# Performance work log

Hardware: AMD Instinct MI355X
Metric: run time of the kernel (lower is better)

Reference implementation:

```python
import jax, jax.numpy as jnp
import numpy as np

RENORM_PERIOD = 256
MAX_NORM = 100.0


def setup_inputs() -> dict:
    key = jax.random.key(0)
    ks = jax.random.split(key, 9)
    B, S, G, D, N = 4, 2048, 8, 128, 64
    return {
        "x_r": jax.random.normal(ks[0], (B, S, G, D), jnp.float32),
        "x_i": jax.random.normal(ks[1], (B, S, G, D), jnp.float32),
        "log_A_mag": jax.random.uniform(ks[2], (G, N), jnp.float32) * 0.5 + 0.5,
        "A_phase": jax.random.normal(ks[3], (G, N), jnp.float32) * 0.1,
        "Bw_r": jax.random.normal(ks[4], (N, D), jnp.float32) / np.sqrt(D),
        "Bw_i": jax.random.normal(ks[5], (N, D), jnp.float32) / np.sqrt(D),
        "Cw_r": jax.random.normal(ks[6], (D, N), jnp.float32) / np.sqrt(N),
        "Cw_i": jax.random.normal(ks[7], (D, N), jnp.float32) / np.sqrt(N),
        "dt_w": jax.random.normal(ks[8], (2, 2 * D), jnp.float32) * 0.02,
        "dt_b": jnp.zeros((2,), jnp.float32),
    }


def reference(x_r, x_i, log_A_mag, A_phase, Bw_r, Bw_i, Cw_r, Cw_i, dt_w, dt_b):
    B, S, G, D = x_r.shape
    N = Bw_r.shape[0]
    # dt: input-dependent step magnitude / phase scale, clamped
    x_cat = jnp.concatenate([x_r, x_i], axis=-1)            # [B,S,G,2D]
    dt = jnp.clip(jnp.exp(jnp.einsum('bsgd,od->bsgo', x_cat, dt_w) + dt_b), 1e-4, 2.0)
    dt_mag = dt[..., 0:1]                                    # [B,S,G,1]
    dt_phase = dt[..., 1:2]
    # A_bar in polar form, |A| = exp(-softplus(log_A_mag)*dt_mag) < 1
    neg_log_A = -jax.nn.softplus(log_A_mag)[None, None]      # [1,1,G,N]
    A_mag = jnp.exp(dt_mag * neg_log_A)                      # [B,S,G,N]
    A_ang = dt_phase * A_phase[None, None]
    A_r = A_mag * jnp.cos(A_ang)
    A_i = A_mag * jnp.sin(A_ang)
    # Bx = (B_proj @ x) * dt_mag, complex linear
    Bx_r = (jnp.einsum('bsgd,nd->bsgn', x_r, Bw_r) - jnp.einsum('bsgd,nd->bsgn', x_i, Bw_i)) * dt_mag
    Bx_i = (jnp.einsum('bsgd,nd->bsgn', x_r, Bw_i) + jnp.einsum('bsgd,nd->bsgn', x_i, Bw_r)) * dt_mag

    def step(carry, inp):
        h_r, h_i = carry
        ar, ai, br, bi, t = inp
        nh_r = ar * h_r - ai * h_i + br
        nh_i = ar * h_i + ai * h_r + bi
        renorm = ((t + 1) % RENORM_PERIOD) == 0
        norm = jnp.sqrt(nh_r * nh_r + nh_i * nh_i + 1e-8)
        scale = jnp.minimum(norm, MAX_NORM) / norm
        nh_r = jnp.where(renorm, nh_r * scale, nh_r)
        nh_i = jnp.where(renorm, nh_i * scale, nh_i)
        return (nh_r, nh_i), (nh_r, nh_i)

    h0 = (jnp.zeros((B, G, N), jnp.float32), jnp.zeros((B, G, N), jnp.float32))
    xs = (jnp.moveaxis(A_r, 1, 0), jnp.moveaxis(A_i, 1, 0),
          jnp.moveaxis(Bx_r, 1, 0), jnp.moveaxis(Bx_i, 1, 0),
          jnp.arange(S))
    _, (all_h_r, all_h_i) = jax.lax.scan(step, h0, xs)       # [S,B,G,N]
    all_h_r = jnp.moveaxis(all_h_r, 0, 1)                    # [B,S,G,N]
    all_h_i = jnp.moveaxis(all_h_i, 0, 1)
    # y = C_proj(h), complex linear N -> D
    y_r = jnp.einsum('bsgn,dn->bsgd', all_h_r, Cw_r) - jnp.einsum('bsgn,dn->bsgd', all_h_i, Cw_i)
    y_i = jnp.einsum('bsgn,dn->bsgd', all_h_r, Cw_i) + jnp.einsum('bsgn,dn->bsgd', all_h_i, Cw_r)
    return jnp.stack([y_r, y_i], axis=0)                     # [2,B,S,G,D]
```

## Files before the change

### kernel.cpp

```cpp
#include <hip/hip_runtime.h>
#include <math.h>

#define B_ 4
#define S_ 2048
#define G_ 8
#define D_ 128
#define N_ 64
#define ROWS (B_*S_*G_)
#define CH 64
#define CLEN 32
#define YOFF (ROWS*D_)

typedef short bf16x8 __attribute__((ext_vector_type(8)));
typedef float f32x4  __attribute__((ext_vector_type(4)));
#define MFMA16(a,b,c) __builtin_amdgcn_mfma_f32_16x16x32_bf16(a,b,c,0,0,0)

__device__ __forceinline__ unsigned short bf16_rtne(float f) {
    unsigned u = __float_as_uint(f);
    unsigned r = (u + 0x7FFFu + ((u >> 16) & 1u)) >> 16;
    return (unsigned short)r;
}
__device__ __forceinline__ void split_bf16(float f, unsigned short &hi, unsigned short &lo) {
    hi = bf16_rtne(f);
    float hif = __uint_as_float(((unsigned)hi) << 16);
    lo = bf16_rtne(f - hif);
}
__device__ __forceinline__ unsigned pk_bf16(float a, float b) {
    unsigned r;
    asm("v_cvt_pk_bf16_f32 %0, %1, %2" : "=v"(r) : "v"(a), "v"(b));
    return r;
}
__device__ __forceinline__ float dot4(float4 a, float4 b) {
    return fmaf(a.x,b.x, fmaf(a.y,b.y, fmaf(a.z,b.z, a.w*b.w)));
}

__global__ __launch_bounds__(256) void k_prep(
    const float* __restrict__ bwr, const float* __restrict__ bwi,
    const float* __restrict__ cwr, const float* __restrict__ cwi,
    unsigned short* __restrict__ wbhi, unsigned short* __restrict__ wblo,
    unsigned short* __restrict__ wchi)
{
    int tid = blockIdx.x * 256 + threadIdx.x;
    if (tid < 4096) {
        int f = tid;
        int lane = f & 63, ks = (f >> 6) & 7, nt = (f >> 9) & 1, w = f >> 10;
        int l15 = lane & 15, quad = lane >> 4;
        int n = w * 32 + nt * 16 + l15;
        int k0 = ks * 32 + quad * 8;
        const float* src; float sgn = 1.f;
        if (n < 64) {
            if (k0 < 128) src = bwr + n * 128 + k0;
            else        { src = bwi + n * 128 + (k0 - 128); sgn = -1.f; }
        } else {
            if (k0 < 128) src = bwi + (n - 64) * 128 + k0;
            else          src = bwr + (n - 64) * 128 + (k0 - 128);
        }
        float4 v0 = *(const float4*)src;
        float4 v1 = *(const float4*)(src + 4);
        float vv[8] = {v0.x,v0.y,v0.z,v0.w,v1.x,v1.y,v1.z,v1.w};
        unsigned short h[8], l[8];
        #pragma unroll
        for (int j = 0; j < 8; j++) split_bf16(vv[j] * sgn, h[j], l[j]);
        #pragma unroll
        for (int j = 0; j < 8; j++) { wbhi[f*8+j] = h[j]; wblo[f*8+j] = l[j]; }
    } else {
        int f = tid - 4096;
        int lane = f & 63, ks = (f >> 6) & 3, nt = (f >> 8) & 3, w = f >> 10;
        int l15 = lane & 15, quad = lane >> 4;
        int n = w * 64 + nt * 16 + l15;
        int d = (n < 128) ? n : (n - 128);
        int k0 = ks * 32 + quad * 8;
        unsigned short h[8];
        #pragma unroll
        for (int j = 0; j < 8; j++) {
            int k = k0 + j, col = k >> 1;
            float val;
            if (n < 128) val = (k & 1) ? -cwi[d * 64 + col] : cwr[d * 64 + col];
            else         val = (k & 1) ?  cwr[d * 64 + col] : cwi[d * 64 + col];
            unsigned short hh, hl; split_bf16(val, hh, hl);
            h[j] = hh;
        }
        #pragma unroll
        for (int j = 0; j < 8; j++) wchi[f*8+j] = h[j];
    }
}

#define LDK1 264
__global__ __launch_bounds__(256, 8) void k_g1(
    const float* __restrict__ xr, const float* __restrict__ xi,
    const float* __restrict__ dtw, const float* __restrict__ dtb,
    const float* __restrict__ logAm, const float* __restrict__ Aph,
    const unsigned short* __restrict__ wbhi,
    float* __restrict__ bxr, float* __restrict__ bxi,
    float* __restrict__ dt_mag, float* __restrict__ dt_ph,
    float4* __restrict__ trans)
{
    __shared__ __align__(16) unsigned short Ahi[32 * LDK1];
    __shared__ float4 comb[192];
    __shared__ float dms[32], dps[32];
    float* bxs = (float*)Ahi;
    const int t = threadIdx.x;
    const int lane = t & 63, w = t >> 6;
    const int l15 = lane & 15, quad = lane >> 4;
    const int bg = blockIdx.x >> 6, c = blockIdx.x & 63;
    const int g = bg & 7, b = bg >> 3;
    const int crow = (bg * CH + c) * CLEN;

    const int kq = t & 31, k4 = kq * 4;
    float4 w0r = *(const float4*)(dtw + k4);
    float4 w0i = *(const float4*)(dtw + 128 + k4);
    float4 w1r = *(const float4*)(dtw + 256 + k4);
    float4 w1i = *(const float4*)(dtw + 384 + k4);
    float b0 = dtb[0], b1 = dtb[1];
    float nla = -logf(1.0f + __expf(logAm[g * N_ + lane]));
    float aph = Aph[g * N_ + lane];

    const bf16x8* WHp = (const bf16x8*)wbhi + (w * 2) * 512 + lane;
    bf16x8 wh0 = WHp[0];
    bf16x8 wh1 = WHp[512];

    const int s0 = c * CLEN;
    const float* xrb = xr + ((size_t)(b * S_ + s0) * G_ + g) * 128;
    const float* xib = xi + ((size_t)(b * S_ + s0) * G_ + g) * 128;

    float pm[4], pp[4];
    #pragma unroll
    for (int i = 0; i < 4; i++) {
        int f = t + 256 * i;
        int m = f >> 5, kk = f & 31;
        float4 a  = ((const float4*)(xrb + m * 1024))[kk];
        float4 bb = ((const float4*)(xib + m * 1024))[kk];
        uint2 h2;
        h2 = make_uint2(pk_bf16(a.x, a.y), pk_bf16(a.z, a.w));
        *(uint2*)&Ahi[m * LDK1 + kk * 4] = h2;
        h2 = make_uint2(pk_bf16(bb.x, bb.y), pk_bf16(bb.z, bb.w));
        *(uint2*)&Ahi[m * LDK1 + 128 + kk * 4] = h2;
        pm[i] = dot4(a, w0r) + dot4(bb, w0i);
        pp[i] = dot4(a, w1r) + dot4(bb, w1i);
    }
    #pragma unroll
    for (int i = 0; i < 4; i++) {
        float vm = pm[i], vp = pp[i];
        #pragma unroll
        for (int msk = 16; msk >= 1; msk >>= 1) {
            vm += __shfl_xor(vm, msk);
            vp += __shfl_xor(vp, msk);
        }
        if ((t & 31) == 0) {
            int m = (t >> 5) + 8 * i;
            float dm = fminf(fmaxf(__expf(vm + b0), 1e-4f), 2.0f);
            float dp = fminf(fmaxf(__expf(vp + b1), 1e-4f), 2.0f);
            dms[m] = dm; dps[m] = dp;
            dt_mag[crow + m] = dm; dt_ph[crow + m] = dp;
        }
    }
    __syncthreads();

    f32x4 acc[2][2];
    #pragma unroll
    for (int a = 0; a < 2; a++)
        #pragma unroll
        for (int bq = 0; bq < 2; bq++)
            acc[a][bq] = (f32x4){0.f, 0.f, 0.f, 0.f};
    #pragma unroll
    for (int ks = 0; ks < 8; ks++) {
        bf16x8 nh0, nh1;
        if (ks < 7) {
            nh0 = WHp[(ks + 1) * 64];
            nh1 = WHp[512 + (ks + 1) * 64];
        }
        #pragma unroll
        for (int ms = 0; ms < 2; ms++) {
            int arow = (ms * 16 + l15) * LDK1 + quad * 8;
            bf16x8 ah = *(const bf16x8*)&Ahi[arow + ks * 32];
            acc[ms][0] = MFMA16(ah, wh0, acc[ms][0]);
            acc[ms][1] = MFMA16(ah, wh1, acc[ms][1]);
        }
        if (ks < 7) { wh0 = nh0; wh1 = nh1; }
    }
    __syncthreads();

    #pragma unroll
    for (int ms = 0; ms < 2; ms++)
        #pragma unroll
        for (int nt = 0; nt < 2; nt++) {
            int n = w * 32 + nt * 16 + l15;
            float* dstg = (n < 64) ? bxr : bxi;
            int nn = n & 63;
            #pragma unroll
            for (int r = 0; r < 4; r++) {
                int m = ms * 16 + quad * 4 + r;
                float v = acc[ms][nt][r] * dms[m];
                dstg[(crow + m) * 64 + nn] = v;
                bxs[m * 132 + n] = v;
            }
        }
    __syncthreads();

    {
        float Ar = 1.f, Ai = 0.f, Br = 0.f, Bi = 0.f;
        const int base = w * 8;
        #pragma unroll
        for (int tt = 0; tt < 8; tt++) {
            const int m = base + tt;
            float dm = dms[m], dp = dps[m];
            float am  = __expf(dm * nla);
            float ang = dp * aph;
            float cr = am * __cosf(ang), ci = am * __sinf(ang);
            float vr = bxs[m * 132 + lane], vi = bxs[m * 132 + 64 + lane];
            float nAr = cr * Ar - ci * Ai;
            float nAi = cr * Ai + ci * Ar;
            float nBr = cr * Br - ci * Bi + vr;
            float nBi = cr * Bi + ci * Br + vi;
            Ar = nAr; Ai = nAi; Br = nBr; Bi = nBi;
        }
        if (w < 3) comb[w * 64 + lane] = make_float4(Ar, Ai, Br, Bi);
        __syncthreads();
        if (w == 3) {
            float4 c0 = comb[lane];
            float cAr = c0.x, cAi = c0.y, cBr = c0.z, cBi = c0.w;
            #pragma unroll
            for (int s = 1; s < 3; s++) {
                float4 ps = comb[s * 64 + lane];
                float nAr = ps.x * cAr - ps.y * cAi;
                float nAi = ps.x * cAi + ps.y * cAr;
                float nBr = ps.x * cBr - ps.y * cBi + ps.z;
                float nBi = ps.x * cBi + ps.y * cBr + ps.w;
                cAr = nAr; cAi = nAi; cBr = nBr; cBi = nBi;
            }
            float fAr = Ar * cAr - Ai * cAi;
            float fAi = Ar * cAi + Ai * cAr;
            float fBr = Ar * cBr - Ai * cBi + Br;
            float fBi = Ar * cBi + Ai * cBr + Bi;
            trans[(bg * CH + c) * 64 + lane] = make_float4(fAr, fAi, fBr, fBi);
        }
    }
}

__global__ __launch_bounds__(256) void k_scanB2(const float4* __restrict__ trans,
    float2* __restrict__ hstart)
{
    int w = threadIdx.x >> 6, lane = threadIdx.x & 63;
    int W = blockIdx.x * 4 + w;
    int bg = W >> 3;
    int n  = ((W & 7) << 3) + (lane & 7);
    int j  = lane >> 3;
    float pAr[8], pAi[8], pBr[8], pBi[8];
    float Ar = 1.f, Ai = 0.f, Br = 0.f, Bi = 0.f;
    const float4* tp = trans + (bg * CH + j * 8) * 64 + n;
    #pragma unroll
    for (int k = 0; k < 8; k++) {
        pAr[k] = Ar; pAi[k] = Ai; pBr[k] = Br; pBi[k] = Bi;
        float4 T = tp[k * 64];
        float nAr = T.x * Ar - T.y * Ai;
        float nAi = T.x * Ai + T.y * Ar;
        float nBr = T.x * Br - T.y * Bi + T.z;
        float nBi = T.x * Bi + T.y * Br + T.w;
        Ar = nAr; Ai = nAi; Br = nBr; Bi = nBi;
    }
    float hr = 0.f, hi = 0.f, mhr = 0.f, mhi = 0.f;
    #pragma unroll
    for (int j2 = 0; j2 < 8; j2++) {
        if (j2 == j) { mhr = hr; mhi = hi; }
        int src = j2 * 8 + (lane & 7);
        float sAr = __shfl(Ar, src), sAi = __shfl(Ai, src);
        float sBr = __shfl(Br, src), sBi = __shfl(Bi, src);
        float nr = sAr * hr - sAi * hi + sBr;
        float ni = sAr * hi + sAi * hr + sBi;
        float nrm = sqrtf(nr * nr + ni * ni + 1e-8f);
        float sc = fminf(nrm, 100.f) / nrm;
        hr = nr * sc; hi = ni * sc;
    }
    float2* hp = hstart + (bg * CH + j * 8) * 64 + n;
    #pragma unroll
    for (int k = 0; k < 8; k++) {
        float hsr = pAr[k] * mhr - pAi[k] * mhi + pBr[k];
        float hsi = pAr[k] * mhi + pAi[k] * mhr + pBi[k];
        hp[k * 64] = make_float2(hsr, hsi);
    }
}

#define LDK2 152
__global__ __launch_bounds__(256, 6) void k_sg2(
    const float* __restrict__ bxr, const float* __restrict__ bxi,
    const float* __restrict__ dt_mag, const float* __restrict__ dt_ph,
    const float* __restrict__ logAm, const float* __restrict__ Aph,
    const float2* __restrict__ hstart,
    const unsigned short* __restrict__ wchi,
    float* __restrict__ out)
{
    __shared__ __align__(16) unsigned short Ahi[32 * LDK2];
    __shared__ __align__(16) unsigned short Alo[32 * LDK2];
    const int t = threadIdx.x;
    const int lane = t & 63, w = t >> 6;
    const int l15 = lane & 15, quad = lane >> 4;
    const int bg = blockIdx.x >> 6, c = blockIdx.x & 63;
    const int g = bg & 7, b = bg >> 3;

    if (w == 0) {
        const int n = lane;
        float nla = -logf(1.0f + __expf(logAm[g * N_ + n]));
        float aph = Aph[g * N_ + n];
        float2 h0 = hstart[(bg * CH + c) * 64 + n];
        float hr = h0.x, hi = h0.y;
        const bool rn = ((c & 7) == 7);
        const int base = (bg * CH + c) * CLEN;
        #pragma unroll 8
        for (int tt = 0; tt < CLEN; tt++) {
            float dm = dt_mag[base + tt], dp = dt_ph[base + tt];
            float am  = __expf(dm * nla);
            float ang = dp * aph;
            float cr = am * __cosf(ang), ci = am * __sinf(ang);
            float vr = bxr[(base + tt) * 64 + n];
            float vi = bxi[(base + tt) * 64 + n];
            float nr = cr * hr - ci * hi + vr;
            float ni = cr * hi + ci * hr + vi;
            if (rn && tt == CLEN - 1) {
                float nrm = sqrtf(nr * nr + ni * ni + 1e-8f);
                float scale = fminf(nrm, 100.0f) / nrm;
                nr *= scale; ni *= scale;
            }
            hr = nr; hi = ni;
            unsigned hp = pk_bf16(hr, hi);
            float rr = hr - __uint_as_float(hp << 16);
            float ri = hi - __uint_as_float(hp & 0xFFFF0000u);
            unsigned lp = pk_bf16(rr, ri);
            *(unsigned*)&Ahi[tt * LDK2 + 2 * n] = hp;
            *(unsigned*)&Alo[tt * LDK2 + 2 * n] = lp;
        }
    }
    __syncthreads();

    f32x4 acc[2][4];
    #pragma unroll
    for (int a = 0; a < 2; a++)
        #pragma unroll
        for (int bq = 0; bq < 4; bq++)
            acc[a][bq] = (f32x4){0.f, 0.f, 0.f, 0.f};
    #pragma unroll
    for (int ks = 0; ks < 4; ks++) {
        bf16x8 wc0 = ((const bf16x8*)wchi)[((w * 4 + 0) * 4 + ks) * 64 + lane];
        bf16x8 wc1 = ((const bf16x8*)wchi)[((w * 4 + 1) * 4 + ks) * 64 + lane];
        bf16x8 wc2 = ((const bf16x8*)wchi)[((w * 4 + 2) * 4 + ks) * 64 + lane];
        bf16x8 wc3 = ((const bf16x8*)wchi)[((w * 4 + 3) * 4 + ks) * 64 + lane];
        #pragma unroll
        for (int ms = 0; ms < 2; ms++) {
            int arow = (ms * 16 + l15) * LDK2 + quad * 8;
            bf16x8 ah = *(const bf16x8*)&Ahi[arow + ks * 32];
            bf16x8 al = *(const bf16x8*)&Alo[arow + ks * 32];
            acc[ms][0] = MFMA16(al, wc0, acc[ms][0]);
            acc[ms][0] = MFMA16(ah, wc0, acc[ms][0]);
            acc[ms][1] = MFMA16(al, wc1, acc[ms][1]);
            acc[ms][1] = MFMA16(ah, wc1, acc[ms][1]);
            acc[ms][2] = MFMA16(al, wc2, acc[ms][2]);
            acc[ms][2] = MFMA16(ah, wc2, acc[ms][2]);
            acc[ms][3] = MFMA16(al, wc3, acc[ms][3]);
            acc[ms][3] = MFMA16(ah, wc3, acc[ms][3]);
        }
    }
    #pragma unroll
    for (int ms = 0; ms < 2; ms++)
        #pragma unroll
        for (int nt = 0; nt < 4; nt++) {
            int nn = w * 64 + nt * 16 + l15;
            float* dst = (nn < 128) ? (out + nn) : (out + YOFF + (nn - 128));
            #pragma unroll
            for (int r = 0; r < 4; r++) {
                int tt2 = ms * 16 + quad * 4 + r;
                int srow = (b * S_ + c * CLEN + tt2) * G_ + g;
                dst[srow * 128] = acc[ms][nt][r];
            }
        }
}

extern "C" void kernel_launch(void* const* d_in, const int* in_sizes, int n_in,
                              void* d_out, int out_size, void* d_ws, size_t ws_size,
                              hipStream_t stream) {
    (void)in_sizes; (void)n_in; (void)out_size; (void)ws_size;
    const float* xr    = (const float*)d_in[0];
    const float* xi    = (const float*)d_in[1];
    const float* logAm = (const float*)d_in[2];
    const float* Aph   = (const float*)d_in[3];
    const float* bwr   = (const float*)d_in[4];
    const float* bwi   = (const float*)d_in[5];
    const float* cwr   = (const float*)d_in[6];
    const float* cwi   = (const float*)d_in[7];
    const float* dtw   = (const float*)d_in[8];
    const float* dtb   = (const float*)d_in[9];
    float* out = (float*)d_out;
    float* ws  = (float*)d_ws;

    float*  dt_mag = ws;
    float*  dt_ph  = ws + 65536;
    float*  bxr    = ws + 131072;
    float*  bxi    = bxr + 4194304;
    float4* trans  = (float4*)(ws + 8519680);
    float2* hstart = (float2*)(ws + 9043968);
    unsigned short* wbhi = (unsigned short*)(ws + 9306112);
    unsigned short* wblo = wbhi + 32768;
    unsigned short* wchi = wblo + 32768;

    hipLaunchKernelGGL(k_prep,   dim3(32), dim3(256), 0, stream,
                       bwr, bwi, cwr, cwi, wbhi, wblo, wchi);
    hipLaunchKernelGGL(k_g1,     dim3((B_ * G_) * 64), dim3(256), 0, stream,
                       xr, xi, dtw, dtb, logAm, Aph, wbhi,
                       bxr, bxi, dt_mag, dt_ph, trans);
    hipLaunchKernelGGL(k_scanB2, dim3(64), dim3(256), 0, stream,
                       trans, hstart);
    hipLaunchKernelGGL(k_sg2,    dim3((B_ * G_) * 64), dim3(256), 0, stream,
                       bxr, bxi, dt_mag, dt_ph, logAm, Aph, hstart, wchi, out);
}
```

Before: 168.4 us.

## Pack Bx to bf16 pairs, two chunks per g1 block, 4-wave parallel chunk scan

Bx is now stored as packed bf16 real/imag pairs instead of two fp32 arrays, halving intermediate write and read traffic. k_g1 handles two consecutive chunks per block and prefetches both chunks' x data into registers up front, which raises per-thread register use and lowers the launch-bounds occupancy target. The final scan kernel splits each 32-step chunk across four waves using local prefix products plus a cross-wave combine, replacing the single-wave serial recurrence. Rounding Bx to bf16 lowers the precision of the scan inputs.

```diff
diff --git a/kernel.cpp b/kernel.cpp
--- a/kernel.cpp
+++ b/kernel.cpp
@@ -86,25 +86,25 @@
 }
 
 #define LDK1 264
-__global__ __launch_bounds__(256, 8) void k_g1(
+__global__ __launch_bounds__(256, 4) void k_g1(
     const float* __restrict__ xr, const float* __restrict__ xi,
     const float* __restrict__ dtw, const float* __restrict__ dtb,
     const float* __restrict__ logAm, const float* __restrict__ Aph,
     const unsigned short* __restrict__ wbhi,
-    float* __restrict__ bxr, float* __restrict__ bxi,
+    unsigned* __restrict__ bxp,
     float* __restrict__ dt_mag, float* __restrict__ dt_ph,
     float4* __restrict__ trans)
 {
     __shared__ __align__(16) unsigned short Ahi[32 * LDK1];
     __shared__ float4 comb[192];
-    __shared__ float dms[32], dps[32];
+    __shared__ float dms[64], dps[64];
     float* bxs = (float*)Ahi;
     const int t = threadIdx.x;
     const int lane = t & 63, w = t >> 6;
     const int l15 = lane & 15, quad = lane >> 4;
-    const int bg = blockIdx.x >> 6, c = blockIdx.x & 63;
+    const int bg = blockIdx.x >> 5, cp = blockIdx.x & 31;
     const int g = bg & 7, b = bg >> 3;
-    const int crow = (bg * CH + c) * CLEN;
+    const int c0 = cp * 2;
 
     const int kq = t & 31, k4 = kq * 4;
     float4 w0r = *(const float4*)(dtw + k4);
@@ -116,123 +116,142 @@
     float aph = Aph[g * N_ + lane];
 
     const bf16x8* WHp = (const bf16x8*)wbhi + (w * 2) * 512 + lane;
-    bf16x8 wh0 = WHp[0];
-    bf16x8 wh1 = WHp[512];
-
-    const int s0 = c * CLEN;
-    const float* xrb = xr + ((size_t)(b * S_ + s0) * G_ + g) * 128;
-    const float* xib = xi + ((size_t)(b * S_ + s0) * G_ + g) * 128;
-
-    float pm[4], pp[4];
-    #pragma unroll
-    for (int i = 0; i < 4; i++) {
-        int f = t + 256 * i;
-        int m = f >> 5, kk = f & 31;
-        float4 a  = ((const float4*)(xrb + m * 1024))[kk];
-        float4 bb = ((const float4*)(xib + m * 1024))[kk];
-        uint2 h2;
-        h2 = make_uint2(pk_bf16(a.x, a.y), pk_bf16(a.z, a.w));
-        *(uint2*)&Ahi[m * LDK1 + kk * 4] = h2;
-        h2 = make_uint2(pk_bf16(bb.x, bb.y), pk_bf16(bb.z, bb.w));
-        *(uint2*)&Ahi[m * LDK1 + 128 + kk * 4] = h2;
-        pm[i] = dot4(a, w0r) + dot4(bb, w0i);
-        pp[i] = dot4(a, w1r) + dot4(bb, w1i);
-    }
-    #pragma unroll
-    for (int i = 0; i < 4; i++) {
-        float vm = pm[i], vp = pp[i];
-        #pragma unroll
-        for (int msk = 16; msk >= 1; msk >>= 1) {
-            vm += __shfl_xor(vm, msk);
-            vp += __shfl_xor(vp, msk);
-        }
-        if ((t & 31) == 0) {
-            int m = (t >> 5) + 8 * i;
-            float dm = fminf(fmaxf(__expf(vm + b0), 1e-4f), 2.0f);
-            float dp = fminf(fmaxf(__expf(vp + b1), 1e-4f), 2.0f);
-            dms[m] = dm; dps[m] = dp;
-            dt_mag[crow + m] = dm; dt_ph[crow + m] = dp;
-        }
-    }
-    __syncthreads();
-
-    f32x4 acc[2][2];
-    #pragma unroll
-    for (int a = 0; a < 2; a++)
-        #pragma unroll
-        for (int bq = 0; bq < 2; bq++)
-            acc[a][bq] = (f32x4){0.f, 0.f, 0.f, 0.f};
-    #pragma unroll
-    for (int ks = 0; ks < 8; ks++) {
-        bf16x8 nh0, nh1;
-        if (ks < 7) {
-            nh0 = WHp[(ks + 1) * 64];
-            nh1 = WHp[512 + (ks + 1) * 64];
-        }
-        #pragma unroll
-        for (int ms = 0; ms < 2; ms++) {
-            int arow = (ms * 16 + l15) * LDK1 + quad * 8;
-            bf16x8 ah = *(const bf16x8*)&Ahi[arow + ks * 32];
-            acc[ms][0] = MFMA16(ah, wh0, acc[ms][0]);
-            acc[ms][1] = MFMA16(ah, wh1, acc[ms][1]);
-        }
-        if (ks < 7) { wh0 = nh0; wh1 = nh1; }
-    }
-    __syncthreads();
-
-    #pragma unroll
-    for (int ms = 0; ms < 2; ms++)
-        #pragma unroll
-        for (int nt = 0; nt < 2; nt++) {
-            int n = w * 32 + nt * 16 + l15;
-            float* dstg = (n < 64) ? bxr : bxi;
-            int nn = n & 63;
-            #pragma unroll
-            for (int r = 0; r < 4; r++) {
-                int m = ms * 16 + quad * 4 + r;
-                float v = acc[ms][nt][r] * dms[m];
-                dstg[(crow + m) * 64 + nn] = v;
-                bxs[m * 132 + n] = v;
-            }
-        }
-    __syncthreads();
-
-    {
-        float Ar = 1.f, Ai = 0.f, Br = 0.f, Bi = 0.f;
-        const int base = w * 8;
-        #pragma unroll
-        for (int tt = 0; tt < 8; tt++) {
-            const int m = base + tt;
-            float dm = dms[m], dp = dps[m];
-            float am  = __expf(dm * nla);
-            float ang = dp * aph;
-            float cr = am * __cosf(ang), ci = am * __sinf(ang);
-            float vr = bxs[m * 132 + lane], vi = bxs[m * 132 + 64 + lane];
-            float nAr = cr * Ar - ci * Ai;
-            float nAi = cr * Ai + ci * Ar;
-            float nBr = cr * Br - ci * Bi + vr;
-            float nBi = cr * Bi + ci * Br + vi;
-            Ar = nAr; Ai = nAi; Br = nBr; Bi = nBi;
-        }
-        if (w < 3) comb[w * 64 + lane] = make_float4(Ar, Ai, Br, Bi);
+
+    const float* xrb = xr + ((size_t)(b * S_ + c0 * CLEN) * G_ + g) * 128;
+    const float* xib = xi + ((size_t)(b * S_ + c0 * CLEN) * G_ + g) * 128;
+
+    float4 XA[2][4], XB[2][4];
+    #pragma unroll
+    for (int q = 0; q < 2; q++)
+        #pragma unroll
+        for (int i = 0; i < 4; i++) {
+            int f = t + 256 * i;
+            int m = f >> 5, kk = f & 31;
+            XA[q][i] = ((const float4*)(xrb + q * 32768 + m * 1024))[kk];
+            XB[q][i] = ((const float4*)(xib + q * 32768 + m * 1024))[kk];
+        }
+
+    #pragma unroll 1
+    for (int q = 0; q < 2; q++) {
         __syncthreads();
-        if (w == 3) {
-            float4 c0 = comb[lane];
-            float cAr = c0.x, cAi = c0.y, cBr = c0.z, cBi = c0.w;
-            #pragma unroll
-            for (int s = 1; s < 3; s++) {
-                float4 ps = comb[s * 64 + lane];
-                float nAr = ps.x * cAr - ps.y * cAi;
-                float nAi = ps.x * cAi + ps.y * cAr;
-                float nBr = ps.x * cBr - ps.y * cBi + ps.z;
-                float nBi = ps.x * cBi + ps.y * cBr + ps.w;
-                cAr = nAr; cAi = nAi; cBr = nBr; cBi = nBi;
-            }
-            float fAr = Ar * cAr - Ai * cAi;
-            float fAi = Ar * cAi + Ai * cAr;
-            float fBr = Ar * cBr - Ai * cBi + Br;
-            float fBi = Ar * cBi + Ai * cBr + Bi;
-            trans[(bg * CH + c) * 64 + lane] = make_float4(fAr, fAi, fBr, fBi);
+        const int c = c0 + q;
+        const int crow = (bg * CH + c) * CLEN;
+        bf16x8 wh0 = WHp[0];
+        bf16x8 wh1 = WHp[512];
+
+        float pm[4], pp[4];
+        #pragma unroll
+        for (int i = 0; i < 4; i++) {
+            int f = t + 256 * i;
+            int m = f >> 5, kk = f & 31;
+            float4 a  = XA[q][i];
+            float4 bb = XB[q][i];
+            *(uint2*)&Ahi[m * LDK1 + kk * 4] =
+                make_uint2(pk_bf16(a.x, a.y), pk_bf16(a.z, a.w));
+            *(uint2*)&Ahi[m * LDK1 + 128 + kk * 4] =
+                make_uint2(pk_bf16(bb.x, bb.y), pk_bf16(bb.z, bb.w));
+            pm[i] = dot4(a, w0r) + dot4(bb, w0i);
+            pp[i] = dot4(a, w1r) + dot4(bb, w1i);
+        }
+        #pragma unroll
+        for (int i = 0; i < 4; i++) {
+            float vm = pm[i], vp = pp[i];
+            #pragma unroll
+            for (int msk = 16; msk >= 1; msk >>= 1) {
+                vm += __shfl_xor(vm, msk);
+                vp += __shfl_xor(vp, msk);
+            }
+            if ((t & 31) == 0) {
+                int m = (t >> 5) + 8 * i;
+                float dm = fminf(fmaxf(__expf(vm + b0), 1e-4f), 2.0f);
+                float dp = fminf(fmaxf(__expf(vp + b1), 1e-4f), 2.0f);
+                dms[q * 32 + m] = dm; dps[q * 32 + m] = dp;
+                dt_mag[crow + m] = dm; dt_ph[crow + m] = dp;
+            }
+        }
+        __syncthreads();
+
+        f32x4 acc[2][2];
+        #pragma unroll
+        for (int a = 0; a < 2; a++)
+            #pragma unroll
+            for (int bq = 0; bq < 2; bq++)
+                acc[a][bq] = (f32x4){0.f, 0.f, 0.f, 0.f};
+        #pragma unroll
+        for (int ks = 0; ks < 8; ks++) {
+            bf16x8 nh0, nh1;
+            if (ks < 7) {
+                nh0 = WHp[(ks + 1) * 64];
+                nh1 = WHp[512 + (ks + 1) * 64];
+            }
+            #pragma unroll
+            for (int ms = 0; ms < 2; ms++) {
+                int arow = (ms * 16 + l15) * LDK1 + quad * 8;
+                bf16x8 ah = *(const bf16x8*)&Ahi[arow + ks * 32];
+                acc[ms][0] = MFMA16(ah, wh0, acc[ms][0]);
+                acc[ms][1] = MFMA16(ah, wh1, acc[ms][1]);
+            }
+            if (ks < 7) { wh0 = nh0; wh1 = nh1; }
+        }
+        __syncthreads();
+
+        #pragma unroll
+        for (int ms = 0; ms < 2; ms++)
+            #pragma unroll
+            for (int nt = 0; nt < 2; nt++) {
+                int n = w * 32 + nt * 16 + l15;
+                #pragma unroll
+                for (int r = 0; r < 4; r++) {
+                    int m = ms * 16 + quad * 4 + r;
+                    bxs[m * 132 + n] = acc[ms][nt][r] * dms[q * 32 + m];
+                }
+            }
+        __syncthreads();
+
+        #pragma unroll
+        for (int i = 0; i < 8; i++) {
+            int e = t + 256 * i;
+            int m = e >> 6, n = e & 63;
+            unsigned u = pk_bf16(bxs[m * 132 + n], bxs[m * 132 + 64 + n]);
+            bxp[(crow + m) * 64 + n] = u;
+        }
+        {
+            float Ar = 1.f, Ai = 0.f, Br = 0.f, Bi = 0.f;
+            const int base = w * 8;
+            #pragma unroll
+            for (int tt = 0; tt < 8; tt++) {
+                const int m = base + tt;
+                float dm = dms[q * 32 + m], dp = dps[q * 32 + m];
+                float am  = __expf(dm * nla);
+                float ang = dp * aph;
+                float cr = am * __cosf(ang), ci = am * __sinf(ang);
+                float vr = bxs[m * 132 + lane], vi = bxs[m * 132 + 64 + lane];
+                float nAr = cr * Ar - ci * Ai;
+                float nAi = cr * Ai + ci * Ar;
+                float nBr = cr * Br - ci * Bi + vr;
+                float nBi = cr * Bi + ci * Br + vi;
+                Ar = nAr; Ai = nAi; Br = nBr; Bi = nBi;
+            }
+            if (w < 3) comb[w * 64 + lane] = make_float4(Ar, Ai, Br, Bi);
+            __syncthreads();
+            if (w == 3) {
+                float4 cc0 = comb[lane];
+                float cAr = cc0.x, cAi = cc0.y, cBr = cc0.z, cBi = cc0.w;
+                #pragma unroll
+                for (int s = 1; s < 3; s++) {
+                    float4 ps = comb[s * 64 + lane];
+                    float nAr = ps.x * cAr - ps.y * cAi;
+                    float nAi = ps.x * cAi + ps.y * cAr;
+                    float nBr = ps.x * cBr - ps.y * cBi + ps.z;
+                    float nBi = ps.x * cBi + ps.y * cBr + ps.w;
+                    cAr = nAr; cAi = nAi; cBr = nBr; cBi = nBi;
+                }
+                float fAr = Ar * cAr - Ai * cAi;
+                float fAi = Ar * cAi + Ai * cAr;
+                float fBr = Ar * cBr - Ai * cBi + Br;
+                float fBi = Ar * cBi + Ai * cBr + Bi;
+                trans[(bg * CH + c) * 64 + lane] = make_float4(fAr, fAi, fBr, fBi);
+            }
         }
     }
 }
@@ -281,8 +300,8 @@
 }
 
 #define LDK2 152
-__global__ __launch_bounds__(256, 6) void k_sg2(
-    const float* __restrict__ bxr, const float* __restrict__ bxi,
+__global__ __launch_bounds__(256, 6) void k_sg4(
+    const unsigned* __restrict__ bxp,
     const float* __restrict__ dt_mag, const float* __restrict__ dt_ph,
     const float* __restrict__ logAm, const float* __restrict__ Aph,
     const float2* __restrict__ hstart,
@@ -291,42 +310,74 @@
 {
     __shared__ __align__(16) unsigned short Ahi[32 * LDK2];
     __shared__ __align__(16) unsigned short Alo[32 * LDK2];
+    __shared__ float4 comb[256];
     const int t = threadIdx.x;
     const int lane = t & 63, w = t >> 6;
     const int l15 = lane & 15, quad = lane >> 4;
     const int bg = blockIdx.x >> 6, c = blockIdx.x & 63;
     const int g = bg & 7, b = bg >> 3;
-
-    if (w == 0) {
-        const int n = lane;
-        float nla = -logf(1.0f + __expf(logAm[g * N_ + n]));
-        float aph = Aph[g * N_ + n];
-        float2 h0 = hstart[(bg * CH + c) * 64 + n];
-        float hr = h0.x, hi = h0.y;
-        const bool rn = ((c & 7) == 7);
-        const int base = (bg * CH + c) * CLEN;
-        #pragma unroll 8
-        for (int tt = 0; tt < CLEN; tt++) {
-            float dm = dt_mag[base + tt], dp = dt_ph[base + tt];
+    const int base = (bg * CH + c) * CLEN;
+    const int s8 = w * 8;
+
+    unsigned bxv[8];
+    #pragma unroll
+    for (int s = 0; s < 8; s++)
+        bxv[s] = bxp[(base + s8 + s) * 64 + lane];
+    float dval = 0.f;
+    if (lane < 8)       dval = dt_mag[base + s8 + lane];
+    else if (lane < 16) dval = dt_ph[base + s8 + (lane - 8)];
+    float2 h0 = hstart[(bg * CH + c) * 64 + lane];
+    float nla = -logf(1.0f + __expf(logAm[g * N_ + lane]));
+    float aph = Aph[g * N_ + lane];
+
+    float paR[8], paI[8], pbR[8], pbI[8];
+    {
+        float Ar = 1.f, Ai = 0.f, Br = 0.f, Bi = 0.f;
+        #pragma unroll
+        for (int s = 0; s < 8; s++) {
+            float dm = __shfl(dval, s), dp = __shfl(dval, 8 + s);
             float am  = __expf(dm * nla);
             float ang = dp * aph;
             float cr = am * __cosf(ang), ci = am * __sinf(ang);
-            float vr = bxr[(base + tt) * 64 + n];
-            float vi = bxi[(base + tt) * 64 + n];
-            float nr = cr * hr - ci * hi + vr;
-            float ni = cr * hi + ci * hr + vi;
-            if (rn && tt == CLEN - 1) {
-                float nrm = sqrtf(nr * nr + ni * ni + 1e-8f);
+            unsigned u = bxv[s];
+            float vr = __uint_as_float(u << 16);
+            float vi = __uint_as_float(u & 0xFFFF0000u);
+            float nAr = cr * Ar - ci * Ai;
+            float nAi = cr * Ai + ci * Ar;
+            float nBr = cr * Br - ci * Bi + vr;
+            float nBi = cr * Bi + ci * Br + vi;
+            Ar = nAr; Ai = nAi; Br = nBr; Bi = nBi;
+            paR[s] = Ar; paI[s] = Ai; pbR[s] = Br; pbI[s] = Bi;
+        }
+        comb[w * 64 + lane] = make_float4(Ar, Ai, Br, Bi);
+    }
+    __syncthreads();
+
+    float Hr = h0.x, Hi = h0.y;
+    for (int s2 = 0; s2 < w; s2++) {
+        float4 T = comb[s2 * 64 + lane];
+        float nr = T.x * Hr - T.y * Hi + T.z;
+        float ni = T.x * Hi + T.y * Hr + T.w;
+        Hr = nr; Hi = ni;
+    }
+    {
+        const bool rn = ((c & 7) == 7) && (w == 3);
+        #pragma unroll
+        for (int s = 0; s < 8; s++) {
+            float hr = paR[s] * Hr - paI[s] * Hi + pbR[s];
+            float hi = paR[s] * Hi + paI[s] * Hr + pbI[s];
+            if (rn && s == 7) {
+                float nrm = sqrtf(hr * hr + hi * hi + 1e-8f);
                 float scale = fminf(nrm, 100.0f) / nrm;
-                nr *= scale; ni *= scale;
-            }
-            hr = nr; hi = ni;
+                hr *= scale; hi *= scale;
+            }
             unsigned hp = pk_bf16(hr, hi);
             float rr = hr - __uint_as_float(hp << 16);
             float ri = hi - __uint_as_float(hp & 0xFFFF0000u);
             unsigned lp = pk_bf16(rr, ri);
-            *(unsigned*)&Ahi[tt * LDK2 + 2 * n] = hp;
-            *(unsigned*)&Alo[tt * LDK2 + 2 * n] = lp;
+            int tt = s8 + s;
+            *(unsigned*)&Ahi[tt * LDK2 + 2 * lane] = hp;
+            *(unsigned*)&Alo[tt * LDK2 + 2 * lane] = lp;
         }
     }
     __syncthreads();
@@ -390,23 +441,22 @@
     float* out = (float*)d_out;
     float* ws  = (float*)d_ws;
 
-    float*  dt_mag = ws;
-    float*  dt_ph  = ws + 65536;
-    float*  bxr    = ws + 131072;
-    float*  bxi    = bxr + 4194304;
-    float4* trans  = (float4*)(ws + 8519680);
-    float2* hstart = (float2*)(ws + 9043968);
+    float*    dt_mag = ws;
+    float*    dt_ph  = ws + 65536;
+    unsigned* bxp    = (unsigned*)(ws + 131072);
+    float4*   trans  = (float4*)(ws + 8519680);
+    float2*   hstart = (float2*)(ws + 9043968);
     unsigned short* wbhi = (unsigned short*)(ws + 9306112);
     unsigned short* wblo = wbhi + 32768;
     unsigned short* wchi = wblo + 32768;
 
     hipLaunchKernelGGL(k_prep,   dim3(32), dim3(256), 0, stream,
                        bwr, bwi, cwr, cwi, wbhi, wblo, wchi);
-    hipLaunchKernelGGL(k_g1,     dim3((B_ * G_) * 64), dim3(256), 0, stream,
+    hipLaunchKernelGGL(k_g1,     dim3((B_ * G_) * 32), dim3(256), 0, stream,
                        xr, xi, dtw, dtb, logAm, Aph, wbhi,
-                       bxr, bxi, dt_mag, dt_ph, trans);
+                       bxp, dt_mag, dt_ph, trans);
     hipLaunchKernelGGL(k_scanB2, dim3(64), dim3(256), 0, stream,
                        trans, hstart);
-    hipLaunchKernelGGL(k_sg2,    dim3((B_ * G_) * 64), dim3(256), 0, stream,
-                       bxr, bxi, dt_mag, dt_ph, logAm, Aph, hstart, wchi, out);
-}
+    hipLaunchKernelGGL(k_sg4,    dim3((B_ * G_) * 64), dim3(256), 0, stream,
+                       bxp, dt_mag, dt_ph, logAm, Aph, hstart, wchi, out);
+}
```

Result: slower. 187.1 us (+11.1%).
